# Kernel tuning notes

Measured on AMD Instinct MI355X. Metric: run time of the kernel, lower is better.

Reference implementation:

```python
import jax, jax.numpy as jnp
from jax import lax
import numpy as np

D_MODEL = 768
D_STATE = 64
D_CONV = 4
EXPAND = 2
D_INNER = EXPAND * D_MODEL          # 1536
HEADDIM = 64
H = D_INNER // HEADDIM              # 24 heads
CONV_DIM = D_INNER + 2 * D_STATE    # 1664 (x, B, C share the conv)
D_IN_PROJ = 2 * D_INNER + 2 * D_STATE + H  # z, xBC, dt
BATCH, SEQ = 4, 4096


def _mamba2(x, in_w, conv_w, conv_b, dt_bias, A_log, Dp, norm_w, out_w):
    """Mamba2 forward (ngroups=1, no in/out-proj bias), faithful to mamba_ssm reference path."""
    Bb, L, _ = x.shape
    zxbcdt = x @ in_w.T                                   # (B,L,D_IN_PROJ)
    z = zxbcdt[..., :D_INNER]
    xBC = zxbcdt[..., D_INNER:D_INNER + CONV_DIM]
    dt = zxbcdt[..., D_INNER + CONV_DIM:]                 # (B,L,H)
    # causal depthwise conv1d over time + SiLU
    xBC = xBC.transpose(0, 2, 1)                          # (B,C,L)
    xBC = lax.conv_general_dilated(xBC, conv_w, (1,), [(D_CONV - 1, 0)],
                                   feature_group_count=CONV_DIM,
                                   dimension_numbers=('NCH', 'OIH', 'NCH'))
    xBC = jax.nn.silu(xBC + conv_b[None, :, None]).transpose(0, 2, 1)
    xs = xBC[..., :D_INNER].reshape(Bb, L, H, HEADDIM)    # (B,L,H,P)
    Bc = xBC[..., D_INNER:D_INNER + D_STATE]              # (B,L,N)
    Cc = xBC[..., D_INNER + D_STATE:]                     # (B,L,N)
    dt = jax.nn.softplus(dt + dt_bias)                    # (B,L,H)
    dA = jnp.exp(dt * (-jnp.exp(A_log)))                  # (B,L,H)
    dtx = dt[..., None] * xs                              # (B,L,H,P)

    def step(h, inp):
        dA_t, dtx_t, B_t, C_t = inp
        h = h * dA_t[:, :, None, None] + jnp.einsum('bhp,bn->bhpn', dtx_t, B_t)
        y = jnp.einsum('bhpn,bn->bhp', h, C_t)
        return h, y

    h0 = jnp.zeros((Bb, H, HEADDIM, D_STATE), x.dtype)
    _, ys = lax.scan(step, h0, (jnp.moveaxis(dA, 1, 0), jnp.moveaxis(dtx, 1, 0),
                                jnp.moveaxis(Bc, 1, 0), jnp.moveaxis(Cc, 1, 0)))
    y = jnp.moveaxis(ys, 0, 1) + Dp[None, None, :, None] * xs  # skip term D*x
    y = y.reshape(Bb, L, D_INNER)
    # RMSNormGated (norm_before_gate=False): gate then normalize
    y = y * jax.nn.silu(z)
    y = y * lax.rsqrt(jnp.mean(y * y, -1, keepdims=True) + 1e-5) * norm_w
    return y @ out_w.T                                    # (B,L,D_MODEL)


def _mamba_params(key, scale=0.02):
    ks = jax.random.split(key, 5)
    in_w = jax.random.normal(ks[0], (D_IN_PROJ, D_MODEL), jnp.float32) * scale
    conv_w = jax.random.normal(ks[1], (CONV_DIM, 1, D_CONV), jnp.float32) * 0.2
    conv_b = jnp.zeros((CONV_DIM,), jnp.float32)
    dt = jax.random.uniform(ks[2], (H,), jnp.float32, 0.001, 0.1)
    dt_bias = dt + jnp.log(-jnp.expm1(-dt))               # inverse softplus
    A_log = jnp.log(jax.random.uniform(ks[3], (H,), jnp.float32, 1.0, 16.0))
    Dp = jnp.ones((H,), jnp.float32)
    norm_w = jnp.ones((D_INNER,), jnp.float32)
    out_w = jax.random.normal(ks[4], (D_MODEL, D_INNER), jnp.float32) * scale
    return in_w, conv_w, conv_b, dt_bias, A_log, Dp, norm_w, out_w


def setup_inputs() -> dict:
    key = jax.random.key(0)
    kx, kf, kb, kw = jax.random.split(key, 4)
    x = jax.random.normal(kx, (BATCH, SEQ, D_MODEL), jnp.float32)
    f = _mamba_params(kf)
    b = _mamba_params(kb)
    fus_w = jax.random.normal(kw, (D_MODEL, 2 * D_MODEL), jnp.float32) * 0.02
    fus_b = jnp.zeros((D_MODEL,), jnp.float32)
    names = ['in_w', 'conv_w', 'conv_b', 'dt_bias', 'A_log', 'D', 'norm_w', 'out_w']
    inp = {'x': x, 'fus_w': fus_w, 'fus_b': fus_b}
    for n, v in zip(names, f):
        inp['f_' + n] = v
    for n, v in zip(names, b):
        inp['b_' + n] = v
    return inp


def reference(x, fus_w, fus_b,
              f_in_w, f_conv_w, f_conv_b, f_dt_bias, f_A_log, f_D, f_norm_w, f_out_w,
              b_in_w, b_conv_w, b_conv_b, b_dt_bias, b_A_log, b_D, b_norm_w, b_out_w):
    out_f = _mamba2(x, f_in_w, f_conv_w, f_conv_b, f_dt_bias, f_A_log, f_D, f_norm_w, f_out_w)
    out_b = jnp.flip(_mamba2(jnp.flip(x, 1), b_in_w, b_conv_w, b_conv_b,
                             b_dt_bias, b_A_log, b_D, b_norm_w, b_out_w), 1)
    out = jnp.concatenate([out_f, out_b], axis=-1)        # (B,L,2*D_MODEL)
    return out @ fus_w.T + fus_b
```

## Files before the change

### kernel.cpp

```cpp
#include <hip/hip_runtime.h>
#include <hip/hip_bf16.h>


#define BATCHN 4
#define SEQL 4096
#define DMODEL 768
#define DINNER 1536
#define DSTATE 64
#define HN 24
#define CONVDIM 1664
#define NROWS_XBC 3200
#define NTOK (BATCHN*SEQL)
#define NCHUNK 64
#define LS 72

typedef short v8s __attribute__((ext_vector_type(8)));
typedef unsigned short v8u __attribute__((ext_vector_type(8)));
typedef float v4f __attribute__((ext_vector_type(4)));
typedef __hip_bfloat16 bf16;

__device__ __forceinline__ int flip_row(int r) {
  return (r & ~4095) | (4095 - (r & 4095));
}
__device__ __forceinline__ float us2f(unsigned short u) {
  return __uint_as_float(((unsigned int)u) << 16);
}
__device__ __forceinline__ unsigned short f2us(float f) {
  bf16 b = __float2bfloat16(f);
  return __builtin_bit_cast(unsigned short, b);
}
__device__ __forceinline__ void async16(const unsigned short* g, unsigned short* l) {
  __builtin_amdgcn_global_load_lds(
      (const __attribute__((address_space(1))) unsigned int*)(const void*)g,
      (__attribute__((address_space(3))) unsigned int*)(void*)l, 16, 0, 0);
}


__global__ void cast_x_kernel(const float* __restrict__ x, bf16* __restrict__ xf) {
  int idx = blockIdx.x * 256 + threadIdx.x;
  xf[idx] = __float2bfloat16(x[idx]);
}

__global__ void cast_kernel(const float* __restrict__ src, bf16* __restrict__ dst) {
  int idx = blockIdx.x * 256 + threadIdx.x;
  dst[idx] = __float2bfloat16(src[idx]);
}

__global__ void cast_strided_kernel(const float* __restrict__ src, bf16* __restrict__ dst,
                                    int cols, int src_stride) {
  int idx = blockIdx.x * 256 + threadIdx.x;
  int j = idx / cols, m = idx % cols;
  dst[idx] = __float2bfloat16(src[(size_t)j * src_stride + m]);
}

__global__ void transpose_ow_kernel(const float* __restrict__ src, bf16* __restrict__ dst) {
  int idx = blockIdx.x * 256 + threadIdx.x;
  int k = idx / DMODEL, c = idx % DMODEL;
  dst[idx] = __float2bfloat16(src[(size_t)c * DINNER + k]);
}

template <bool OUT_BF16>
__global__ __launch_bounds__(256) void gemm_lds(
    const bf16* __restrict__ A, const bf16* __restrict__ B, void* __restrict__ C,
    int K, int ldc, int flip_a, int flip_c, int accum, const float* __restrict__ bias) {
  __shared__ unsigned short sA[128 * 32];
  __shared__ unsigned short sB[128 * 32];
  int tid = threadIdx.x;
  int wave = tid >> 6, lane = tid & 63;
  int l15 = lane & 15, quad = lane >> 4;
  int m0 = blockIdx.x * 128, n0 = blockIdx.y * 128;
  int mw = (wave >> 1) * 64, nw = (wave & 1) * 64;

  int srow = wave * 32 + (lane >> 2);
  int scol = (lane & 3) * 8;
  const unsigned short* Ap = (const unsigned short*)A;
  const unsigned short* Bp = (const unsigned short*)B;
  int ar0 = m0 + srow, ar1 = m0 + srow + 16;
  if (flip_a) { ar0 = flip_row(ar0); ar1 = flip_row(ar1); }
  const unsigned short* ga0 = Ap + (size_t)ar0 * K + scol;
  const unsigned short* ga1 = Ap + (size_t)ar1 * K + scol;
  const unsigned short* gb0 = Bp + (size_t)(n0 + srow) * K + scol;
  const unsigned short* gb1 = Bp + (size_t)(n0 + srow + 16) * K + scol;
  unsigned short* lA0 = &sA[(wave * 32) * 32];
  unsigned short* lA1 = &sA[(wave * 32 + 16) * 32];
  unsigned short* lB0 = &sB[(wave * 32) * 32];
  unsigned short* lB1 = &sB[(wave * 32 + 16) * 32];

  v4f acc[4][4];
#pragma unroll
  for (int i = 0; i < 4; i++)
#pragma unroll
    for (int j = 0; j < 4; j++) acc[i][j] = {0.f, 0.f, 0.f, 0.f};

  for (int k0 = 0; k0 < K; k0 += 32) {
    async16(ga0 + k0, lA0);
    async16(ga1 + k0, lA1);
    async16(gb0 + k0, lB0);
    async16(gb1 + k0, lB1);
    __syncthreads();
    v8s af[4], bfr[4];
#pragma unroll
    for (int i = 0; i < 4; i++)
      af[i] = *(const v8s*)&sA[(mw + i * 16 + l15) * 32 + quad * 8];
#pragma unroll
    for (int j = 0; j < 4; j++)
      bfr[j] = *(const v8s*)&sB[(nw + j * 16 + l15) * 32 + quad * 8];
#pragma unroll
    for (int i = 0; i < 4; i++)
#pragma unroll
      for (int j = 0; j < 4; j++)
        acc[i][j] = __builtin_amdgcn_mfma_f32_16x16x32_bf16(af[i], bfr[j], acc[i][j], 0, 0, 0);
    __syncthreads();
  }

  float bv[4];
#pragma unroll
  for (int j = 0; j < 4; j++) bv[j] = bias ? bias[n0 + nw + j * 16 + l15] : 0.f;

#pragma unroll
  for (int i = 0; i < 4; i++) {
#pragma unroll
    for (int r = 0; r < 4; r++) {
      int row = m0 + mw + i * 16 + quad * 4 + r;
      int orow = flip_c ? flip_row(row) : row;
#pragma unroll
      for (int j = 0; j < 4; j++) {
        int col = n0 + nw + j * 16 + l15;
        float v = acc[i][j][r] + bv[j];
        size_t off = (size_t)orow * ldc + col;
        if (OUT_BF16) {
          ((bf16*)C)[off] = __float2bfloat16(v);
        } else {
          float* Cf = (float*)C;
          if (accum) v += Cf[off];
          Cf[off] = v;
        }
      }
    }
  }
}

__global__ __launch_bounds__(256) void dt_fused_kernel(
    const float* __restrict__ x,
    const float* __restrict__ in_w0, const float* __restrict__ in_w1,
    const float* __restrict__ dt_bias0, const float* __restrict__ dt_bias1,
    const float* __restrict__ A_log0, const float* __restrict__ A_log1,
    float* __restrict__ dt0, float* __restrict__ dl0,
    float* __restrict__ dt1, float* __restrict__ dl1) {
  __shared__ float sXT[64][128];
  __shared__ float sW[24][64];
  int tid = threadIdx.x;
  int tok2 = tid & 63, cg = tid >> 6;
  int dir = blockIdx.y;
  int tok_base = blockIdx.x * 128;

  int st_tok = tid >> 1, st_k0 = (tid & 1) * 32;
  const float* xg = x + (size_t)(tok_base + st_tok) * DMODEL + st_k0;
  const float* wb = dir ? in_w1 : in_w0;
  const float* wrow = wb + (size_t)NROWS_XBC * DMODEL;

  float acc0[6], acc1[6];
#pragma unroll
  for (int c = 0; c < 6; c++) { acc0[c] = 0.f; acc1[c] = 0.f; }

#pragma unroll 1
  for (int kc = 0; kc < 12; kc++) {
#pragma unroll
    for (int i = 0; i < 8; i++) {
      v4f v = *(const v4f*)(xg + kc * 64 + i * 4);
#pragma unroll
      for (int j = 0; j < 4; j++) sXT[st_k0 + i * 4 + j][st_tok] = v[j];
    }
    for (int i = tid; i < 24 * 16; i += 256) {
      int col = i >> 4, k4 = i & 15;
      *(v4f*)&sW[col][k4 * 4] =
          *(const v4f*)(wrow + (size_t)col * DMODEL + kc * 64 + k4 * 4);
    }
    __syncthreads();
#pragma unroll 2
    for (int k4 = 0; k4 < 16; k4++) {
      float xa[4], xb[4];
#pragma unroll
      for (int j = 0; j < 4; j++) {
        xa[j] = sXT[k4 * 4 + j][tok2];
        xb[j] = sXT[k4 * 4 + j][tok2 + 64];
      }
#pragma unroll
      for (int c = 0; c < 6; c++) {
        v4f wv = *(const v4f*)&sW[cg * 6 + c][k4 * 4];
#pragma unroll
        for (int j = 0; j < 4; j++) {
          acc0[c] = fmaf(xa[j], wv[j], acc0[c]);
          acc1[c] = fmaf(xb[j], wv[j], acc1[c]);
        }
      }
    }
    __syncthreads();
  }

  const float* dtB = dir ? dt_bias1 : dt_bias0;
  const float* Alg = dir ? A_log1 : A_log0;
  float* dto = dir ? dt1 : dt0;
  float* dlo = dir ? dl1 : dl0;
#pragma unroll
  for (int t = 0; t < 2; t++) {
    int r = tok_base + t * 64 + tok2;
    size_t row = dir ? (size_t)flip_row(r) : (size_t)r;
#pragma unroll
    for (int c = 0; c < 6; c++) {
      int h = cg * 6 + c;
      float v = (t ? acc1[c] : acc0[c]) + dtB[h];
      float dtv = (v > 20.f) ? v : log1pf(expf(v));
      dto[row * HN + h] = dtv;
      dlo[row * HN + h] = -dtv * expf(Alg[h]);
    }
  }
}

__global__ void conv_bc_kernel(const bf16* __restrict__ xbcr,
                               const float* __restrict__ conv_w,
                               const float* __restrict__ conv_b,
                               bf16* __restrict__ Bblob, bf16* __restrict__ Cblob) {
  int idx = blockIdx.x * 256 + threadIdx.x;
  int token = idx >> 7, ch7 = idx & 127;
  int b = token >> 12, l = token & 4095, c = l >> 6, s = l & 63;
  int ch = 1536 + ch7;
  float acc = conv_b[ch];
  const float* w4 = conv_w + ch * 4;
#pragma unroll
  for (int j = 0; j < 4; j++) {
    int ls = l - 3 + j;
    if (ls >= 0)
      acc += __bfloat162float(xbcr[(size_t)((b << 12) | ls) * CONVDIM + ch]) * w4[j];
  }
  float v = acc / (1.f + __expf(-acc));
  size_t base = ((size_t)((b * 64 + c) * 64 + s)) * 64;
  if (ch7 < 64) Bblob[base + ch7] = __float2bfloat16(v);
  else          Cblob[base + (ch7 - 64)] = __float2bfloat16(v);
}

__global__ __launch_bounds__(256) void chunk_intra_kernel(
    const bf16* __restrict__ xbcr, const bf16* __restrict__ Bblob,
    const bf16* __restrict__ Cblob, const float* __restrict__ conv_w,
    const float* __restrict__ conv_b, const float* __restrict__ dtb,
    const float* __restrict__ dlb, const float* __restrict__ Dp,
    bf16* __restrict__ Yblob, bf16* __restrict__ Gblob, float* __restrict__ laq) {
  int blk = blockIdx.x;
  int c = blk & 63, bh = blk >> 6;
  int h = bh % HN, b = bh / HN;
  int tid = threadIdx.x, lane = tid & 63, wv = tid >> 6;
  int l15 = lane & 15, quad = lane >> 4;
  int tok0 = b * SEQL + c * 64;

  __shared__ unsigned short sXT[64][LS];
  __shared__ unsigned short sB [64][LS];
  __shared__ unsigned short sBT[64][LS];
  __shared__ unsigned short sC [64][LS];
  __shared__ union { unsigned short rawX[67][66]; unsigned short W[64][LS]; } sU;
  __shared__ float sla[64], sdt[64], sdG[64];

  for (int i = tid; i < 67 * 64; i += 256) {
    int p = i & 63, s67 = i >> 6;
    int l = c * 64 + s67 - 3;
    unsigned short v = 0;
    if (l >= 0)
      v = ((const unsigned short*)xbcr)[(size_t)(b * SEQL + l) * CONVDIM + h * 64 + p];
    sU.rawX[s67][p] = v;
  }
  {
    const v8u* gB = (const v8u*)((const unsigned short*)Bblob + ((size_t)(b * 64 + c)) * 4096);
    const v8u* gC = (const v8u*)((const unsigned short*)Cblob + ((size_t)(b * 64 + c)) * 4096);
    int r0 = tid >> 3, g0 = tid & 7;
#pragma unroll
    for (int it = 0; it < 2; it++) {
      int row = r0 + it * 32;
      *(v8u*)&sB[row][g0 * 8] = gB[row * 8 + g0];
      *(v8u*)&sC[row][g0 * 8] = gC[row * 8 + g0];
    }
  }
  if (wv == 0) {
    float dtv = dtb[(size_t)(tok0 + lane) * HN + h];
    float lg = dlb[(size_t)(tok0 + lane) * HN + h];
#pragma unroll
    for (int d = 1; d < 64; d <<= 1) {
      float o = __shfl_up(lg, d);
      if (lane >= d) lg += o;
    }
    sla[lane] = lg;
    sdt[lane] = dtv;
    float la63 = __shfl(lg, 63);
    sdG[lane] = __expf(la63 - lg) * dtv;
    if (lane == 63) laq[blk] = __expf(la63);
  }
  __syncthreads();

  float Dh = Dp[h];
  {
    int s = tid & 63;
#pragma unroll
    for (int it = 0; it < 16; it++) {
      int p = (tid >> 6) + it * 4;
      int ch = h * 64 + p;
      float acc = conv_b[ch];
      const float* w4 = conv_w + ch * 4;
#pragma unroll
      for (int j = 0; j < 4; j++) acc += us2f(sU.rawX[s + j][p]) * w4[j];
      sXT[p][s] = f2us(acc / (1.f + __expf(-acc)));
    }
#pragma unroll
    for (int it = 0; it < 16; it++) {
      int n = (tid >> 6) + it * 4;
      sBT[n][s] = f2us(us2f(sB[s][n]) * sdG[s]);
    }
  }
  __syncthreads();

  {
    v4f acc[4];
#pragma unroll
    for (int j = 0; j < 4; j++) acc[j] = {0.f, 0.f, 0.f, 0.f};
#pragma unroll
    for (int k0 = 0; k0 < 2; k0++) {
      v8s a = *(const v8s*)&sC[16 * wv + l15][k0 * 32 + quad * 8];
#pragma unroll
      for (int j = 0; j < 4; j++) {
        v8s bb = *(const v8s*)&sB[16 * j + l15][k0 * 32 + quad * 8];
        acc[j] = __builtin_amdgcn_mfma_f32_16x16x32_bf16(a, bb, acc[j], 0, 0, 0);
      }
    }
    float lat[4];
#pragma unroll
    for (int r = 0; r < 4; r++) lat[r] = sla[16 * wv + quad * 4 + r];
#pragma unroll
    for (int j = 0; j < 4; j++) {
      int s = 16 * j + l15;
      float las = sla[s], dts = sdt[s];
#pragma unroll
      for (int r = 0; r < 4; r++) {
        int t = 16 * wv + quad * 4 + r;
        float w = (s <= t) ? __expf(lat[r] - las) * dts * acc[j][r] : 0.f;
        sU.W[t][s] = f2us(w);
      }
    }
  }
  __syncthreads();

  {
    v4f ya[4], ga[4];
#pragma unroll
    for (int j = 0; j < 4; j++) {
      ya[j] = {0.f, 0.f, 0.f, 0.f};
      ga[j] = {0.f, 0.f, 0.f, 0.f};
    }
#pragma unroll
    for (int k0 = 0; k0 < 2; k0++) {
      v8s aw = *(const v8s*)&sU.W[16 * wv + l15][k0 * 32 + quad * 8];
      v8s ax = *(const v8s*)&sXT[16 * wv + l15][k0 * 32 + quad * 8];
#pragma unroll
      for (int j = 0; j < 4; j++) {
        v8s bx = *(const v8s*)&sXT[16 * j + l15][k0 * 32 + quad * 8];
        v8s bt = *(const v8s*)&sBT[16 * j + l15][k0 * 32 + quad * 8];
        ya[j] = __builtin_amdgcn_mfma_f32_16x16x32_bf16(aw, bx, ya[j], 0, 0, 0);
        ga[j] = __builtin_amdgcn_mfma_f32_16x16x32_bf16(ax, bt, ga[j], 0, 0, 0);
      }
    }
#pragma unroll
    for (int j = 0; j < 4; j++) {
      int col = 16 * j + l15;
#pragma unroll
      for (int r = 0; r < 4; r++) {
        int row = 16 * wv + quad * 4 + r;
        float yv = ya[j][r] + Dh * us2f(sXT[col][row]);
        sB[row][col] = f2us(yv);
        sC[row][col] = f2us(ga[j][r]);
      }
    }
  }
  __syncthreads();

  {
    unsigned int* gY = (unsigned int*)(Yblob + (size_t)blk * 4096);
    unsigned int* gG = (unsigned int*)(Gblob + (size_t)blk * 4096);
#pragma unroll
    for (int it = 0; it < 8; it++) {
      int d = tid + it * 256;
      int row = d >> 5, col2 = d & 31;
      gY[row * 32 + col2] = *(const unsigned int*)&sB[row][col2 * 2];
      gG[row * 32 + col2] = *(const unsigned int*)&sC[row][col2 * 2];
    }
  }
}

__global__ __launch_bounds__(256) void state_scan_kernel(
    bf16* __restrict__ blob, const float* __restrict__ laq) {
  int bh = blockIdx.x;
  int tid = threadIdx.x;
  size_t base = (size_t)bh * 64 * 4096 + (size_t)(tid >> 2) * 64 + (size_t)(tid & 3) * 16;
  float S[16];
#pragma unroll
  for (int i = 0; i < 16; i++) S[i] = 0.f;
  for (int c = 0; c < 64; c++) {
    float q = laq[bh * 64 + c];
    unsigned short* gp = (unsigned short*)blob + base + (size_t)c * 4096;
    v8u ga = ((v8u*)gp)[0], gb = ((v8u*)gp)[1];
    v8u pa, pb;
#pragma unroll
    for (int i = 0; i < 8; i++) {
      pa[i] = f2us(S[i]);
      pb[i] = f2us(S[8 + i]);
    }
    ((v8u*)gp)[0] = pa;
    ((v8u*)gp)[1] = pb;
#pragma unroll
    for (int i = 0; i < 8; i++) {
      S[i] = q * S[i] + us2f(ga[i]);
      S[8 + i] = q * S[8 + i] + us2f(gb[i]);
    }
  }
}

__global__ __launch_bounds__(256) void chunk_inter_kernel(
    const bf16* __restrict__ Cblob, const float* __restrict__ dlb,
    const bf16* __restrict__ blob, bf16* __restrict__ Yblob) {
  int blk = blockIdx.x;
  int c = blk & 63, bh = blk >> 6;
  int h = bh % HN, b = bh / HN;
  int tid = threadIdx.x, lane = tid & 63, wv = tid >> 6;
  int l15 = lane & 15, quad = lane >> 4;
  int tok0 = b * SEQL + c * 64;

  __shared__ unsigned short sC[64][LS];
  __shared__ unsigned short sY[64][LS];
  __shared__ float sel[64];

  {
    const v8u* gC = (const v8u*)((const unsigned short*)Cblob + ((size_t)(b * 64 + c)) * 4096);
    int r0 = tid >> 3, g0 = tid & 7;
#pragma unroll
    for (int it = 0; it < 2; it++) {
      int row = r0 + it * 32;
      *(v8u*)&sC[row][g0 * 8] = gC[row * 8 + g0];
    }
  }
  if (wv == 0) {
    float lg = dlb[(size_t)(tok0 + lane) * HN + h];
#pragma unroll
    for (int d = 1; d < 64; d <<= 1) {
      float o = __shfl_up(lg, d);
      if (lane >= d) lg += o;
    }
    sel[lane] = __expf(lg);
  }
  __syncthreads();
  {
    v4f acc[4];
#pragma unroll
    for (int j = 0; j < 4; j++) acc[j] = {0.f, 0.f, 0.f, 0.f};
    const unsigned short* gS = (const unsigned short*)blob + (size_t)blk * 4096;
#pragma unroll
    for (int k0 = 0; k0 < 2; k0++) {
      v8s a = *(const v8s*)&sC[16 * wv + l15][k0 * 32 + quad * 8];
#pragma unroll
      for (int j = 0; j < 4; j++) {
        v8s bS = *(const v8s*)(gS + (size_t)(16 * j + l15) * 64 + k0 * 32 + quad * 8);
        acc[j] = __builtin_amdgcn_mfma_f32_16x16x32_bf16(a, bS, acc[j], 0, 0, 0);
      }
    }
    float selt[4];
#pragma unroll
    for (int r = 0; r < 4; r++) selt[r] = sel[16 * wv + quad * 4 + r];
#pragma unroll
    for (int j = 0; j < 4; j++)
#pragma unroll
      for (int r = 0; r < 4; r++)
        sY[16 * wv + quad * 4 + r][16 * j + l15] = f2us(selt[r] * acc[j][r]);
  }
  __syncthreads();
  {
    unsigned int* gY = (unsigned int*)(Yblob + (size_t)blk * 4096);
#pragma unroll
    for (int it = 0; it < 8; it++) {
      int d = tid + it * 256;
      int row = d >> 5, col2 = d & 31;
      unsigned int old = gY[row * 32 + col2];
      float lo = us2f((unsigned short)(old & 0xffff)) + us2f(sY[row][col2 * 2]);
      float hi = us2f((unsigned short)(old >> 16)) + us2f(sY[row][col2 * 2 + 1]);
      gY[row * 32 + col2] = (unsigned int)f2us(lo) | ((unsigned int)f2us(hi) << 16);
    }
  }
}

__global__ __launch_bounds__(256) void norm_kernel(
    const bf16* __restrict__ Yblob, const bf16* __restrict__ z,
    const float* __restrict__ norm_w, bf16* __restrict__ out) {
  int token = blockIdx.x;
  int tid = threadIdx.x;
  int b = token >> 12, l = token & 4095, c = l >> 6, t = l & 63;
  const bf16* zp = z + (size_t)token * DINNER;
  float vals[6];
  float ss = 0.f;
#pragma unroll
  for (int i = 0; i < 6; i++) {
    int ch = tid + i * 256;
    int h = ch >> 6, p = ch & 63;
    size_t yi = ((((size_t)(b * HN + h)) * 64 + c) * 64 + t) * 64 + p;
    float yv = __bfloat162float(Yblob[yi]);
    float zv = __bfloat162float(zp[ch]);
    float g = zv / (1.f + __expf(-zv));
    float v = yv * g;
    vals[i] = v;
    ss += v * v;
  }
  for (int off = 32; off > 0; off >>= 1) ss += __shfl_down(ss, off);
  __shared__ float sred[4];
  if ((tid & 63) == 0) sred[tid >> 6] = ss;
  __syncthreads();
  float tot = sred[0] + sred[1] + sred[2] + sred[3];
  float scale = rsqrtf(tot / (float)DINNER + 1e-5f);
#pragma unroll
  for (int i = 0; i < 6; i++) {
    int ch = tid + i * 256;
    out[(size_t)token * DINNER + ch] = __float2bfloat16(vals[i] * scale * norm_w[ch]);
  }
}

extern "C" void kernel_launch(void* const* d_in, const int* in_sizes, int n_in,
                              void* d_out, int out_size, void* d_ws, size_t ws_size,
                              hipStream_t stream) {
  const float* x = (const float*)d_in[0];
  const float* fus_w = (const float*)d_in[1];
  const float* fus_b = (const float*)d_in[2];
  const float* in_w[2] = {(const float*)d_in[3], (const float*)d_in[11]};
  const float* conv_w[2] = {(const float*)d_in[4], (const float*)d_in[12]};
  const float* conv_b[2] = {(const float*)d_in[5], (const float*)d_in[13]};
  const float* dt_bias[2] = {(const float*)d_in[6], (const float*)d_in[14]};
  const float* A_log[2] = {(const float*)d_in[7], (const float*)d_in[15]};
  const float* Dp[2] = {(const float*)d_in[8], (const float*)d_in[16]};
  const float* norm_w[2] = {(const float*)d_in[9], (const float*)d_in[17]};
  const float* out_w[2] = {(const float*)d_in[10], (const float*)d_in[18]};
  (void)in_sizes; (void)n_in;

  char* ws = (char*)d_ws;
  size_t off = 0;
  auto alloc = [&](size_t bytes) {
    size_t o = off;
    off = (off + bytes + 255) & ~(size_t)255;
    return o;
  };
  bf16* x_bf  = (bf16*)(ws + alloc((size_t)NTOK * DMODEL * 2));
  bf16* w_in  = (bf16*)(ws + alloc((size_t)NROWS_XBC * DMODEL * 2));
  bf16* wf1   = (bf16*)(ws + alloc((size_t)DMODEL * DMODEL * 2));
  bf16* owT   = (bf16*)(ws + alloc((size_t)DINNER * DMODEL * 2));
  bf16* wc    = (bf16*)(ws + alloc((size_t)DMODEL * DINNER * 2));
  bf16* xbcr  = (bf16*)(ws + alloc((size_t)NTOK * CONVDIM * 2));
  float* dtb0 = (float*)(ws + alloc((size_t)NTOK * HN * 4));
  float* dlb0 = (float*)(ws + alloc((size_t)NTOK * HN * 4));
  float* dtb1 = (float*)(ws + alloc((size_t)NTOK * HN * 4));
  float* dlb1 = (float*)(ws + alloc((size_t)NTOK * HN * 4));
  float* laq  = (float*)(ws + alloc((size_t)BATCHN * HN * NCHUNK * 4));
  bf16* Bblob = (bf16*)(ws + alloc((size_t)NTOK * DSTATE * 2));
  bf16* Cblob = (bf16*)(ws + alloc((size_t)NTOK * DSTATE * 2));
  bf16* Gblob = (bf16*)(ws + alloc((size_t)NTOK * DINNER * 2));
  bf16* Yblob = (bf16*)(ws + alloc((size_t)NTOK * DINNER * 2));
  bf16* zbuf  = Gblob;
  bf16* ynorm = xbcr;
  float* dtbs[2] = {dtb0, dtb1};
  float* dlbs[2] = {dlb0, dlb1};

  if (ws_size < off) {
    hipMemsetAsync(d_out, 0, (size_t)out_size * 4, stream);
    return;
  }

  cast_x_kernel<<<(NTOK * DMODEL) / 256, 256, 0, stream>>>(x, x_bf);
  dt_fused_kernel<<<dim3(NTOK / 128, 2), 256, 0, stream>>>(
      x, in_w[0], in_w[1], dt_bias[0], dt_bias[1], A_log[0], A_log[1],
      dtb0, dlb0, dtb1, dlb1);

  for (int dir = 0; dir < 2; dir++) {
    cast_kernel<<<(NROWS_XBC * DMODEL) / 256, 256, 0, stream>>>(in_w[dir], w_in);
    gemm_lds<true><<<dim3(NTOK / 128, CONVDIM / 128), 256, 0, stream>>>(
        x_bf, w_in + (size_t)DINNER * DMODEL, xbcr, DMODEL, CONVDIM, dir, 0, 0, nullptr);
    conv_bc_kernel<<<(NTOK * 128) / 256, 256, 0, stream>>>(
        xbcr, conv_w[dir], conv_b[dir], Bblob, Cblob);
    chunk_intra_kernel<<<BATCHN * HN * NCHUNK, 256, 0, stream>>>(
        xbcr, Bblob, Cblob, conv_w[dir], conv_b[dir], dtbs[dir], dlbs[dir], Dp[dir],
        Yblob, Gblob, laq);
    state_scan_kernel<<<BATCHN * HN, 256, 0, stream>>>(Gblob, laq);
    chunk_inter_kernel<<<BATCHN * HN * NCHUNK, 256, 0, stream>>>(Cblob, dlbs[dir], Gblob, Yblob);
    gemm_lds<true><<<dim3(NTOK / 128, DINNER / 128), 256, 0, stream>>>(
        x_bf, w_in, zbuf, DMODEL, DINNER, dir, 0, 0, nullptr);
    norm_kernel<<<NTOK, 256, 0, stream>>>(Yblob, zbuf, norm_w[dir], ynorm);
    cast_strided_kernel<<<(DMODEL * DMODEL) / 256, 256, 0, stream>>>(
        fus_w + dir * DMODEL, wf1, DMODEL, 2 * DMODEL);
    transpose_ow_kernel<<<(DINNER * DMODEL) / 256, 256, 0, stream>>>(out_w[dir], owT);
    gemm_lds<true><<<dim3(DMODEL / 128, DINNER / 128), 256, 0, stream>>>(
        wf1, owT, wc, DMODEL, DINNER, 0, 0, 0, nullptr);
    gemm_lds<false><<<dim3(NTOK / 128, DMODEL / 128), 256, 0, stream>>>(
        ynorm, wc, d_out, DINNER, DMODEL, 0, dir, dir, dir == 0 ? fus_b : nullptr);
  }
}
```

Measured before the change: 1.047 ms.

## Vectorize global loads and stores across cast, conv, chunk and norm kernels

The cast, transpose, conv_bc, chunk_intra, chunk_inter and norm kernels now move 4 to 8 elements per thread using wide vector loads and stores, and their grid sizes are reduced to match. The chunk_intra conv staging pads rawX rows to 72 so 16-byte LDS stores stay aligned. s_setprio hints are wrapped around the MFMA loops. The goal is fewer memory instructions and better coalescing in the memory-bound elementwise stages. In exchange each thread does more work, and the grids assume sizes divisible by the vector widths.

```diff
diff --git a/kernel.cpp b/kernel.cpp
--- a/kernel.cpp
+++ b/kernel.cpp
@@ -17,6 +17,7 @@
 typedef short v8s __attribute__((ext_vector_type(8)));
 typedef unsigned short v8u __attribute__((ext_vector_type(8)));
 typedef float v4f __attribute__((ext_vector_type(4)));
+typedef unsigned int v2u32 __attribute__((ext_vector_type(2)));
 typedef __hip_bfloat16 bf16;
 
 __device__ __forceinline__ int flip_row(int r) {
@@ -38,25 +39,44 @@
 
 __global__ void cast_x_kernel(const float* __restrict__ x, bf16* __restrict__ xf) {
   int idx = blockIdx.x * 256 + threadIdx.x;
-  xf[idx] = __float2bfloat16(x[idx]);
+  v4f v = *(const v4f*)(x + (size_t)idx * 4);
+  v2u32 o;
+  o[0] = (unsigned int)f2us(v[0]) | ((unsigned int)f2us(v[1]) << 16);
+  o[1] = (unsigned int)f2us(v[2]) | ((unsigned int)f2us(v[3]) << 16);
+  *(v2u32*)((unsigned short*)xf + (size_t)idx * 4) = o;
 }
 
 __global__ void cast_kernel(const float* __restrict__ src, bf16* __restrict__ dst) {
   int idx = blockIdx.x * 256 + threadIdx.x;
-  dst[idx] = __float2bfloat16(src[idx]);
+  v4f v = *(const v4f*)(src + (size_t)idx * 4);
+  v2u32 o;
+  o[0] = (unsigned int)f2us(v[0]) | ((unsigned int)f2us(v[1]) << 16);
+  o[1] = (unsigned int)f2us(v[2]) | ((unsigned int)f2us(v[3]) << 16);
+  *(v2u32*)((unsigned short*)dst + (size_t)idx * 4) = o;
 }
 
 __global__ void cast_strided_kernel(const float* __restrict__ src, bf16* __restrict__ dst,
                                     int cols, int src_stride) {
-  int idx = blockIdx.x * 256 + threadIdx.x;
-  int j = idx / cols, m = idx % cols;
-  dst[idx] = __float2bfloat16(src[(size_t)j * src_stride + m]);
+  int idx4 = (blockIdx.x * 256 + threadIdx.x) * 4;
+  int j = idx4 / cols, m = idx4 % cols;
+  v4f v = *(const v4f*)(src + (size_t)j * src_stride + m);
+  v2u32 o;
+  o[0] = (unsigned int)f2us(v[0]) | ((unsigned int)f2us(v[1]) << 16);
+  o[1] = (unsigned int)f2us(v[2]) | ((unsigned int)f2us(v[3]) << 16);
+  *(v2u32*)((unsigned short*)dst + idx4) = o;
 }
 
 __global__ void transpose_ow_kernel(const float* __restrict__ src, bf16* __restrict__ dst) {
-  int idx = blockIdx.x * 256 + threadIdx.x;
-  int k = idx / DMODEL, c = idx % DMODEL;
-  dst[idx] = __float2bfloat16(src[(size_t)c * DINNER + k]);
+  int idx4 = (blockIdx.x * 256 + threadIdx.x) * 4;
+  int k = idx4 / DMODEL, c0 = idx4 % DMODEL;
+  unsigned short u[4];
+#pragma unroll
+  for (int i = 0; i < 4; i++)
+    u[i] = f2us(src[(size_t)(c0 + i) * DINNER + k]);
+  v2u32 o;
+  o[0] = (unsigned int)u[0] | ((unsigned int)u[1] << 16);
+  o[1] = (unsigned int)u[2] | ((unsigned int)u[3] << 16);
+  *(v2u32*)((unsigned short*)dst + idx4) = o;
 }
 
 template <bool OUT_BF16>
@@ -222,21 +242,33 @@
                                const float* __restrict__ conv_b,
                                bf16* __restrict__ Bblob, bf16* __restrict__ Cblob) {
   int idx = blockIdx.x * 256 + threadIdx.x;
-  int token = idx >> 7, ch7 = idx & 127;
+  int token = idx >> 4, oct = idx & 15;
   int b = token >> 12, l = token & 4095, c = l >> 6, s = l & 63;
-  int ch = 1536 + ch7;
-  float acc = conv_b[ch];
-  const float* w4 = conv_w + ch * 4;
+  int ch0 = 1536 + oct * 8;
+  const unsigned short* xp = (const unsigned short*)xbcr;
+  v8u tv[4];
 #pragma unroll
   for (int j = 0; j < 4; j++) {
     int ls = l - 3 + j;
+    v8u z = {0, 0, 0, 0, 0, 0, 0, 0};
+    tv[j] = z;
     if (ls >= 0)
-      acc += __bfloat162float(xbcr[(size_t)((b << 12) | ls) * CONVDIM + ch]) * w4[j];
-  }
-  float v = acc / (1.f + __expf(-acc));
+      tv[j] = *(const v8u*)(xp + (size_t)((b << 12) | ls) * CONVDIM + ch0);
+  }
+  v8u ov;
+#pragma unroll
+  for (int e = 0; e < 8; e++) {
+    int ch = ch0 + e;
+    const float* w4 = conv_w + ch * 4;
+    float acc = conv_b[ch];
+#pragma unroll
+    for (int j = 0; j < 4; j++) acc += us2f(tv[j][e]) * w4[j];
+    ov[e] = f2us(acc / (1.f + __expf(-acc)));
+  }
   size_t base = ((size_t)((b * 64 + c) * 64 + s)) * 64;
-  if (ch7 < 64) Bblob[base + ch7] = __float2bfloat16(v);
-  else          Cblob[base + (ch7 - 64)] = __float2bfloat16(v);
+  int ch7 = oct * 8;
+  if (ch7 < 64) *(v8u*)((unsigned short*)Bblob + base + ch7) = ov;
+  else          *(v8u*)((unsigned short*)Cblob + base + ch7 - 64) = ov;
 }
 
 __global__ __launch_bounds__(256) void chunk_intra_kernel(
@@ -256,16 +288,17 @@
   __shared__ unsigned short sB [64][LS];
   __shared__ unsigned short sBT[64][LS];
   __shared__ unsigned short sC [64][LS];
-  __shared__ union { unsigned short rawX[67][66]; unsigned short W[64][LS]; } sU;
+  __shared__ union { unsigned short rawX[67][72]; unsigned short W[64][LS]; } sU;
   __shared__ float sla[64], sdt[64], sdG[64];
 
-  for (int i = tid; i < 67 * 64; i += 256) {
-    int p = i & 63, s67 = i >> 6;
-    int l = c * 64 + s67 - 3;
-    unsigned short v = 0;
+  for (int i = tid; i < 536; i += 256) {
+    int r = i >> 3, j = i & 7;
+    int l = c * 64 + r - 3;
+    v8u v = {0, 0, 0, 0, 0, 0, 0, 0};
     if (l >= 0)
-      v = ((const unsigned short*)xbcr)[(size_t)(b * SEQL + l) * CONVDIM + h * 64 + p];
-    sU.rawX[s67][p] = v;
+      v = *(const v8u*)((const unsigned short*)xbcr +
+                        (size_t)(b * SEQL + l) * CONVDIM + h * 64 + j * 8);
+    *(v8u*)&sU.rawX[r][j * 8] = v;
   }
   {
     const v8u* gB = (const v8u*)((const unsigned short*)Bblob + ((size_t)(b * 64 + c)) * 4096);
@@ -296,20 +329,26 @@
 
   float Dh = Dp[h];
   {
-    int s = tid & 63;
+    int s = lane;
+#pragma unroll
+    for (int o = 0; o < 2; o++) {
+      int p0 = (wv * 2 + o) * 8;
+      v8u r0 = *(const v8u*)&sU.rawX[s + 0][p0];
+      v8u r1 = *(const v8u*)&sU.rawX[s + 1][p0];
+      v8u r2 = *(const v8u*)&sU.rawX[s + 2][p0];
+      v8u r3 = *(const v8u*)&sU.rawX[s + 3][p0];
+#pragma unroll
+      for (int pp = 0; pp < 8; pp++) {
+        int ch = h * 64 + p0 + pp;
+        const float* w4 = conv_w + ch * 4;
+        float acc = conv_b[ch] + us2f(r0[pp]) * w4[0] + us2f(r1[pp]) * w4[1] +
+                    us2f(r2[pp]) * w4[2] + us2f(r3[pp]) * w4[3];
+        sXT[p0 + pp][s] = f2us(acc / (1.f + __expf(-acc)));
+      }
+    }
 #pragma unroll
     for (int it = 0; it < 16; it++) {
-      int p = (tid >> 6) + it * 4;
-      int ch = h * 64 + p;
-      float acc = conv_b[ch];
-      const float* w4 = conv_w + ch * 4;
-#pragma unroll
-      for (int j = 0; j < 4; j++) acc += us2f(sU.rawX[s + j][p]) * w4[j];
-      sXT[p][s] = f2us(acc / (1.f + __expf(-acc)));
-    }
-#pragma unroll
-    for (int it = 0; it < 16; it++) {
-      int n = (tid >> 6) + it * 4;
+      int n = wv + it * 4;
       sBT[n][s] = f2us(us2f(sB[s][n]) * sdG[s]);
     }
   }
@@ -319,6 +358,7 @@
     v4f acc[4];
 #pragma unroll
     for (int j = 0; j < 4; j++) acc[j] = {0.f, 0.f, 0.f, 0.f};
+    __builtin_amdgcn_s_setprio(1);
 #pragma unroll
     for (int k0 = 0; k0 < 2; k0++) {
       v8s a = *(const v8s*)&sC[16 * wv + l15][k0 * 32 + quad * 8];
@@ -328,6 +368,7 @@
         acc[j] = __builtin_amdgcn_mfma_f32_16x16x32_bf16(a, bb, acc[j], 0, 0, 0);
       }
     }
+    __builtin_amdgcn_s_setprio(0);
     float lat[4];
 #pragma unroll
     for (int r = 0; r < 4; r++) lat[r] = sla[16 * wv + quad * 4 + r];
@@ -352,6 +393,7 @@
       ya[j] = {0.f, 0.f, 0.f, 0.f};
       ga[j] = {0.f, 0.f, 0.f, 0.f};
     }
+    __builtin_amdgcn_s_setprio(1);
 #pragma unroll
     for (int k0 = 0; k0 < 2; k0++) {
       v8s aw = *(const v8s*)&sU.W[16 * wv + l15][k0 * 32 + quad * 8];
@@ -364,6 +406,7 @@
         ga[j] = __builtin_amdgcn_mfma_f32_16x16x32_bf16(ax, bt, ga[j], 0, 0, 0);
       }
     }
+    __builtin_amdgcn_s_setprio(0);
 #pragma unroll
     for (int j = 0; j < 4; j++) {
       int col = 16 * j + l15;
@@ -379,14 +422,14 @@
   __syncthreads();
 
   {
-    unsigned int* gY = (unsigned int*)(Yblob + (size_t)blk * 4096);
-    unsigned int* gG = (unsigned int*)(Gblob + (size_t)blk * 4096);
-#pragma unroll
-    for (int it = 0; it < 8; it++) {
-      int d = tid + it * 256;
-      int row = d >> 5, col2 = d & 31;
-      gY[row * 32 + col2] = *(const unsigned int*)&sB[row][col2 * 2];
-      gG[row * 32 + col2] = *(const unsigned int*)&sC[row][col2 * 2];
+    v8u* gY = (v8u*)(Yblob + (size_t)blk * 4096);
+    v8u* gG = (v8u*)(Gblob + (size_t)blk * 4096);
+#pragma unroll
+    for (int it = 0; it < 2; it++) {
+      int i = tid + it * 256;
+      int row = i >> 3, j = i & 7;
+      gY[row * 8 + j] = *(const v8u*)&sB[row][j * 8];
+      gG[row * 8 + j] = *(const v8u*)&sC[row][j * 8];
     }
   }
 }
@@ -457,6 +500,7 @@
 #pragma unroll
     for (int j = 0; j < 4; j++) acc[j] = {0.f, 0.f, 0.f, 0.f};
     const unsigned short* gS = (const unsigned short*)blob + (size_t)blk * 4096;
+    __builtin_amdgcn_s_setprio(1);
 #pragma unroll
     for (int k0 = 0; k0 < 2; k0++) {
       v8s a = *(const v8s*)&sC[16 * wv + l15][k0 * 32 + quad * 8];
@@ -466,6 +510,7 @@
         acc[j] = __builtin_amdgcn_mfma_f32_16x16x32_bf16(a, bS, acc[j], 0, 0, 0);
       }
     }
+    __builtin_amdgcn_s_setprio(0);
     float selt[4];
 #pragma unroll
     for (int r = 0; r < 4; r++) selt[r] = sel[16 * wv + quad * 4 + r];
@@ -477,15 +522,17 @@
   }
   __syncthreads();
   {
-    unsigned int* gY = (unsigned int*)(Yblob + (size_t)blk * 4096);
-#pragma unroll
-    for (int it = 0; it < 8; it++) {
-      int d = tid + it * 256;
-      int row = d >> 5, col2 = d & 31;
-      unsigned int old = gY[row * 32 + col2];
-      float lo = us2f((unsigned short)(old & 0xffff)) + us2f(sY[row][col2 * 2]);
-      float hi = us2f((unsigned short)(old >> 16)) + us2f(sY[row][col2 * 2 + 1]);
-      gY[row * 32 + col2] = (unsigned int)f2us(lo) | ((unsigned int)f2us(hi) << 16);
+    v8u* gY = (v8u*)(Yblob + (size_t)blk * 4096);
+#pragma unroll
+    for (int it = 0; it < 2; it++) {
+      int i = tid + it * 256;
+      int row = i >> 3, j = i & 7;
+      v8u old = gY[row * 8 + j];
+      v8u add = *(const v8u*)&sY[row][j * 8];
+      v8u outv;
+#pragma unroll
+      for (int e = 0; e < 8; e++) outv[e] = f2us(us2f(old[e]) + us2f(add[e]));
+      gY[row * 8 + j] = outv;
     }
   }
 }
@@ -496,20 +543,26 @@
   int token = blockIdx.x;
   int tid = threadIdx.x;
   int b = token >> 12, l = token & 4095, c = l >> 6, t = l & 63;
-  const bf16* zp = z + (size_t)token * DINNER;
+  const unsigned short* zp = (const unsigned short*)z + (size_t)token * DINNER;
   float vals[6];
   float ss = 0.f;
 #pragma unroll
-  for (int i = 0; i < 6; i++) {
-    int ch = tid + i * 256;
-    int h = ch >> 6, p = ch & 63;
-    size_t yi = ((((size_t)(b * HN + h)) * 64 + c) * 64 + t) * 64 + p;
-    float yv = __bfloat162float(Yblob[yi]);
-    float zv = __bfloat162float(zp[ch]);
-    float g = zv / (1.f + __expf(-zv));
-    float v = yv * g;
-    vals[i] = v;
-    ss += v * v;
+  for (int i = 0; i < 3; i++) {
+    int q = tid + i * 256;
+    int ch = q * 2;
+    int hh = ch >> 6, p = ch & 63;
+    size_t yi = ((((size_t)(b * HN + hh)) * 64 + c) * 64 + t) * 64 + p;
+    unsigned int yv2 = *(const unsigned int*)((const unsigned short*)Yblob + yi);
+    unsigned int zv2 = *(const unsigned int*)(zp + ch);
+#pragma unroll
+    for (int e = 0; e < 2; e++) {
+      float yv = us2f((unsigned short)((yv2 >> (16 * e)) & 0xffff));
+      float zv = us2f((unsigned short)((zv2 >> (16 * e)) & 0xffff));
+      float g = zv / (1.f + __expf(-zv));
+      float v = yv * g;
+      vals[i * 2 + e] = v;
+      ss += v * v;
+    }
   }
   for (int off = 32; off > 0; off >>= 1) ss += __shfl_down(ss, off);
   __shared__ float sred[4];
@@ -518,9 +571,13 @@
   float tot = sred[0] + sred[1] + sred[2] + sred[3];
   float scale = rsqrtf(tot / (float)DINNER + 1e-5f);
 #pragma unroll
-  for (int i = 0; i < 6; i++) {
-    int ch = tid + i * 256;
-    out[(size_t)token * DINNER + ch] = __float2bfloat16(vals[i] * scale * norm_w[ch]);
+  for (int i = 0; i < 3; i++) {
+    int q = tid + i * 256;
+    int ch = q * 2;
+    unsigned int o =
+        (unsigned int)f2us(vals[i * 2] * scale * norm_w[ch]) |
+        ((unsigned int)f2us(vals[i * 2 + 1] * scale * norm_w[ch + 1]) << 16);
+    *(unsigned int*)((unsigned short*)out + (size_t)token * DINNER + ch) = o;
   }
 }
 
@@ -572,16 +629,16 @@
     return;
   }
 
-  cast_x_kernel<<<(NTOK * DMODEL) / 256, 256, 0, stream>>>(x, x_bf);
+  cast_x_kernel<<<(NTOK * DMODEL) / 1024, 256, 0, stream>>>(x, x_bf);
   dt_fused_kernel<<<dim3(NTOK / 128, 2), 256, 0, stream>>>(
       x, in_w[0], in_w[1], dt_bias[0], dt_bias[1], A_log[0], A_log[1],
       dtb0, dlb0, dtb1, dlb1);
 
   for (int dir = 0; dir < 2; dir++) {
-    cast_kernel<<<(NROWS_XBC * DMODEL) / 256, 256, 0, stream>>>(in_w[dir], w_in);
+    cast_kernel<<<(NROWS_XBC * DMODEL) / 1024, 256, 0, stream>>>(in_w[dir], w_in);
     gemm_lds<true><<<dim3(NTOK / 128, CONVDIM / 128), 256, 0, stream>>>(
         x_bf, w_in + (size_t)DINNER * DMODEL, xbcr, DMODEL, CONVDIM, dir, 0, 0, nullptr);
-    conv_bc_kernel<<<(NTOK * 128) / 256, 256, 0, stream>>>(
+    conv_bc_kernel<<<(NTOK * 16) / 256, 256, 0, stream>>>(
         xbcr, conv_w[dir], conv_b[dir], Bblob, Cblob);
     chunk_intra_kernel<<<BATCHN * HN * NCHUNK, 256, 0, stream>>>(
         xbcr, Bblob, Cblob, conv_w[dir], conv_b[dir], dtbs[dir], dlbs[dir], Dp[dir],
@@ -591,9 +648,9 @@
     gemm_lds<true><<<dim3(NTOK / 128, DINNER / 128), 256, 0, stream>>>(
         x_bf, w_in, zbuf, DMODEL, DINNER, dir, 0, 0, nullptr);
     norm_kernel<<<NTOK, 256, 0, stream>>>(Yblob, zbuf, norm_w[dir], ynorm);
-    cast_strided_kernel<<<(DMODEL * DMODEL) / 256, 256, 0, stream>>>(
+    cast_strided_kernel<<<(DMODEL * DMODEL) / 1024, 256, 0, stream>>>(
         fus_w + dir * DMODEL, wf1, DMODEL, 2 * DMODEL);
-    transpose_ow_kernel<<<(DINNER * DMODEL) / 256, 256, 0, stream>>>(out_w[dir], owT);
+    transpose_ow_kernel<<<(DINNER * DMODEL) / 1024, 256, 0, stream>>>(out_w[dir], owT);
     gemm_lds<true><<<dim3(DMODEL / 128, DINNER / 128), 256, 0, stream>>>(
         wf1, owT, wc, DMODEL, DINNER, 0, 0, 0, nullptr);
     gemm_lds<false><<<dim3(NTOK / 128, DMODEL / 128), 256, 0, stream>>>(
```

Measured after the change: 959.6 us. -8.4%, faster.
